# Kernel tuning notes

Hardware: AMD Instinct MI355X
Metric: run time of the kernel (lower is better)

The kernel has to match this reference:

```python
import jax, jax.numpy as jnp
import numpy as np

V = 5000   # vocab (input_size == output_size)
H = 512    # hidden_size
N = 8      # batch
T = 2048   # sequence length


def setup_inputs() -> dict:
    key = jax.random.key(0)
    ks = jax.random.split(key, 6)
    x = jax.random.randint(ks[0], (N, T), 0, V)
    # embedding table (acts as W_xh: xh = E[token])
    E = jax.random.normal(ks[1], (V, H), dtype=jnp.float32) * 0.02
    # hidden Linear(H, H): torch convention W [out, in], y = h @ W.T + b
    Wh = jax.random.normal(ks[2], (H, H), dtype=jnp.float32) * (1.0 / np.sqrt(H))
    bh = jnp.zeros((H,), dtype=jnp.float32)
    # out Linear(H, V)
    Wo = jax.random.normal(ks[3], (V, H), dtype=jnp.float32) * (1.0 / np.sqrt(H))
    bo = jnp.zeros((V,), dtype=jnp.float32)
    return {"x": x, "E": E, "Wh": Wh, "bh": bh, "Wo": Wo, "bo": bo}


def reference(x, E, Wh, bh, Wo, bo):
    n = x.shape[0]
    h0 = jnp.zeros((n, H), dtype=E.dtype)  # h=None -> zeros, broadcast over batch

    def step(h, x_t):
        xh = E[x_t]                              # [N, H] embedding lookup
        h = jnp.tanh(xh + h @ Wh.T + bh)         # [N, H]
        z = h @ Wo.T + bo                        # [N, V]
        return h, jax.nn.softmax(z, axis=-1)

    h_final, y = jax.lax.scan(step, h0, x.T)     # y: [T, N, V]
    return jnp.transpose(y, (1, 0, 2)), h_final  # ([N, T, V], [N, H])
```

## Files before the change

kernel.cpp:

```cpp
#include <hip/hip_runtime.h>
#include <cstdint>
#include <cmath>

#define V_SZ 5000
#define H_SZ 512
#define N_SZ 8
#define T_LEN 2048
#define NTV (81920000LL)

typedef __bf16 bf16;
typedef __bf16 bf16x2 __attribute__((ext_vector_type(2)));
typedef __bf16 bf16x8 __attribute__((ext_vector_type(8)));
typedef float  f32x4  __attribute__((ext_vector_type(4)));
typedef int    i32x4  __attribute__((ext_vector_type(4)));

__device__ __forceinline__ void llc_store16(void* p, i32x4 v) {
    asm volatile("global_store_dwordx4 %0, %1, off sc0 sc1"
                 :: "v"(p), "v"(v) : "memory");
}
__device__ __forceinline__ void llc_load2(const void* p0, const void* p1,
                                          i32x4& a, i32x4& b) {
    asm volatile("global_load_dwordx4 %0, %2, off sc0 sc1\n\t"
                 "global_load_dwordx4 %1, %3, off sc0 sc1\n\t"
                 "s_waitcnt vmcnt(0)"
                 : "=&v"(a), "=&v"(b)
                 : "v"(p0), "v"(p1)
                 : "memory");
}

__global__ __launch_bounds__(256) void prep_wo(const float* __restrict__ Wo,
                                               bf16* __restrict__ Wo16) {
    int idx = (blockIdx.x * 256 + threadIdx.x) * 4;
    if (idx >= 5120 * 512) return;
    float4 v = make_float4(0.f, 0.f, 0.f, 0.f);
    if (idx < V_SZ * H_SZ) v = *(const float4*)(Wo + idx);
    Wo16[idx + 0] = (bf16)v.x;
    Wo16[idx + 1] = (bf16)v.y;
    Wo16[idx + 2] = (bf16)v.z;
    Wo16[idx + 3] = (bf16)v.w;
}

__global__ __launch_bounds__(1024, 1) void rnn_rec3(
        const int*   __restrict__ x,
        const float* __restrict__ E,
        const float* __restrict__ Wh,
        const float* __restrict__ bh,
        char*        __restrict__ Hx,
        bf16*        __restrict__ Hall,
        float*       __restrict__ out) {
    __shared__ bf16  Abuf[2 * 16 * 520];
    __shared__ float Ds[16 * 272];

    const int tid  = threadIdx.x;
    const int blk  = blockIdx.x;
    const int lane = tid & 63;
    const int wv   = tid >> 6;
    const int l15  = lane & 15;
    const int quad = lane >> 4;
    const int j0   = blk * 128;

    for (int i = tid; i < 2 * 16 * 520; i += 1024) Abuf[i] = (bf16)0.f;

    bf16x8 wf[16];
    {
        const float* wrow = Wh + (size_t)(j0 + (wv & 7) * 16 + l15) * H_SZ;
        const bool lo_pass = (wv >= 8);
#pragma unroll
        for (int kt = 0; kt < 16; ++kt) {
            const float* p = wrow + kt * 32 + quad * 8;
            bf16x8 f;
#pragma unroll
            for (int i = 0; i < 8; ++i) {
                float v = p[i];
                bf16 hi = (bf16)v;
                f[i] = lo_pass ? (bf16)(v - (float)hi) : hi;
            }
            wf[kt] = f;
        }
    }

    const int rn = tid >> 7, rj = tid & 127;
    const float bhv = bh[j0 + rj];
    const int jt = rj >> 4, jl = rj & 15;
    const int* xrow = x + rn * T_LEN;

    int off0, off1, dst0, dst1;
    bool has1 = (tid < 512);
    {
        int c0 = tid;
        int rbp0 = c0 >> 9, cc0 = c0 & 511;
        int rb0 = rbp0 + (rbp0 >= blk);
        off0 = (rb0 * 512 + cc0) * 16;
        dst0 = (cc0 >> 6) * 520 + rb0 * 128 + 2 * (cc0 & 63);
        int c1 = has1 ? (tid + 1024) : c0;
        int rbp1 = c1 >> 9, cc1 = c1 & 511;
        int rb1 = rbp1 + (rbp1 >= blk);
        off1 = (rb1 * 512 + cc1) * 16;
        dst1 = (cc1 >> 6) * 520 + rb1 * 128 + 2 * (cc1 & 63);
    }

    int budget = 1 << 22;
    __syncthreads();

    for (int t = 0; t < T_LEN; ++t) {
        const float ev = E[(size_t)xrow[t] * H_SZ + j0 + rj];

        if (t > 0) {
            const char* base = Hx + (size_t)(t & 1) * 32768;
            bf16* An = Abuf + (t & 1) * (16 * 520);
            const int wtag = t;
            const void* p0 = base + off0;
            const void* p1 = base + off1;
            bool need0 = true, need1 = has1;
            while (need0 | need1) {
                i32x4 a, b;
                llc_load2(p0, p1, a, b);
                if (need0 & (a.y == wtag) & (a.w == wtag)) {
                    float h0 = __int_as_float(a.x), h1 = __int_as_float(a.z);
                    bf16 hi0 = (bf16)h0, hi1 = (bf16)h1;
                    *(bf16x2*)(An + dst0) = (bf16x2){hi0, hi1};
                    *(bf16x2*)(An + 8 * 520 + dst0) =
                        (bf16x2){(bf16)(h0 - (float)hi0), (bf16)(h1 - (float)hi1)};
                    need0 = false;
                }
                if (need1 & (b.y == wtag) & (b.w == wtag)) {
                    float h0 = __int_as_float(b.x), h1 = __int_as_float(b.z);
                    bf16 hi0 = (bf16)h0, hi1 = (bf16)h1;
                    *(bf16x2*)(An + dst1) = (bf16x2){hi0, hi1};
                    *(bf16x2*)(An + 8 * 520 + dst1) =
                        (bf16x2){(bf16)(h0 - (float)hi0), (bf16)(h1 - (float)hi1)};
                    need1 = false;
                }
                if (--budget < 0) break;
            }
        }
        __syncthreads();

        {
            const bf16* Ab = Abuf + (t & 1) * (16 * 520);
            f32x4 acc = {}, acc2 = {};
#pragma unroll
            for (int kt = 0; kt < 16; kt += 2) {
                bf16x8 af0 = *(const bf16x8*)(Ab + l15 * 520 + kt * 32 + quad * 8);
                bf16x8 af1 = *(const bf16x8*)(Ab + l15 * 520 + (kt + 1) * 32 + quad * 8);
                acc  = __builtin_amdgcn_mfma_f32_16x16x32_bf16(af0, wf[kt],     acc,  0, 0, 0);
                acc2 = __builtin_amdgcn_mfma_f32_16x16x32_bf16(af1, wf[kt + 1], acc2, 0, 0, 0);
            }
            acc += acc2;
#pragma unroll
            for (int r = 0; r < 4; ++r)
                Ds[wv * 272 + (quad * 4 + r) * 17 + l15] = acc[r];
        }
        __syncthreads();

        {
            float s = Ds[jt * 272 + rn * 17 + jl]
                    + Ds[jt * 272 + (rn + 8) * 17 + jl]
                    + Ds[(jt + 8) * 272 + rn * 17 + jl]
                    + Ds[(jt + 8) * 272 + (rn + 8) * 17 + jl];
            float h = tanhf(s + bhv + ev);

            float hodd = __shfl_xor(h, 1, 64);
            if (((tid & 1) == 0) & (t < T_LEN - 1)) {
                i32x4 ch;
                ch.x = __float_as_int(h);
                ch.y = t + 1;
                ch.z = __float_as_int(hodd);
                ch.w = t + 1;
                char* dstp = Hx + (size_t)((t + 1) & 1) * 32768
                           + (size_t)(blk * 512 + rn * 64 + (rj >> 1)) * 16;
                llc_store16(dstp, ch);
            }

            Hall[((size_t)rn * T_LEN + t) * H_SZ + j0 + rj] = (bf16)h;
            bf16 hi = (bf16)h;
            bf16* An = Abuf + ((t + 1) & 1) * (16 * 520);
            An[rn * 520 + j0 + rj] = hi;
            An[(rn + 8) * 520 + j0 + rj] = (bf16)(h - (float)hi);
            if (t == T_LEN - 1) out[NTV + rn * H_SZ + j0 + rj] = h;
        }
    }
}

#define LDK 72
__global__ __launch_bounds__(256) void gemm_bt(
        const bf16* __restrict__ A,
        const bf16* __restrict__ B,
        const float* __restrict__ bo,
        float* __restrict__ C) {
    __shared__ bf16 As[128 * LDK];
    __shared__ bf16 Bs[128 * LDK];

    const int tid  = threadIdx.x;
    const int lane = tid & 63;
    const int wid  = tid >> 6;
    const int wm   = wid & 1, wn = wid >> 1;
    const int bm   = blockIdx.y, bn = blockIdx.x;
    const int rowA0 = bm * 128, rowB0 = bn * 128;

    const int quad = lane >> 4;
    const int l15  = lane & 15;

    f32x4 acc[4][4] = {};

    for (int kt = 0; kt < H_SZ / 64; ++kt) {
        __syncthreads();
#pragma unroll
        for (int i = 0; i < 4; ++i) {
            int p = i * 256 + tid;
            int r = p >> 3, c8 = p & 7;
            bf16x8 va = *(const bf16x8*)(A + (size_t)(rowA0 + r) * H_SZ + kt * 64 + c8 * 8);
            *(bf16x8*)(As + r * LDK + c8 * 8) = va;
            bf16x8 vb = *(const bf16x8*)(B + (size_t)(rowB0 + r) * H_SZ + kt * 64 + c8 * 8);
            *(bf16x8*)(Bs + r * LDK + c8 * 8) = vb;
        }
        __syncthreads();

#pragma unroll
        for (int ks = 0; ks < 2; ++ks) {
            bf16x8 af[4], bfr[4];
            const int koff = ks * 32 + quad * 8;
#pragma unroll
            for (int mi = 0; mi < 4; ++mi) {
                int row = wm * 64 + mi * 16 + l15;
                af[mi] = *(const bf16x8*)(As + row * LDK + koff);
            }
#pragma unroll
            for (int ni = 0; ni < 4; ++ni) {
                int row = wn * 64 + ni * 16 + l15;
                bfr[ni] = *(const bf16x8*)(Bs + row * LDK + koff);
            }
#pragma unroll
            for (int mi = 0; mi < 4; ++mi)
#pragma unroll
                for (int ni = 0; ni < 4; ++ni)
                    acc[mi][ni] = __builtin_amdgcn_mfma_f32_16x16x32_bf16(
                        af[mi], bfr[ni], acc[mi][ni], 0, 0, 0);
        }
    }

#pragma unroll
    for (int mi = 0; mi < 4; ++mi) {
#pragma unroll
        for (int ni = 0; ni < 4; ++ni) {
            int vcol = rowB0 + wn * 64 + ni * 16 + l15;
            if (vcol >= V_SZ) continue;
            float bias = bo[vcol];
#pragma unroll
            for (int r = 0; r < 4; ++r) {
                int m = rowA0 + wm * 64 + mi * 16 + quad * 4 + r;
                C[(size_t)m * V_SZ + vcol] = acc[mi][ni][r] + bias;
            }
        }
    }
}

__global__ __launch_bounds__(256) void softmax_rows(float* __restrict__ z) {
    __shared__ float buf[5008];
    __shared__ float red[8];
    const int tid = threadIdx.x;
    const int lane = tid & 63;
    const int wid = tid >> 6;
    const size_t base = (size_t)blockIdx.x * V_SZ;

    float lm = -3.4e38f;
    for (int i = tid; i < V_SZ; i += 256) {
        float v = z[base + i];
        buf[i] = v;
        lm = fmaxf(lm, v);
    }
#pragma unroll
    for (int o = 32; o; o >>= 1) lm = fmaxf(lm, __shfl_down(lm, o, 64));
    if (lane == 0) red[wid] = lm;
    __syncthreads();
    const float m = fmaxf(fmaxf(red[0], red[1]), fmaxf(red[2], red[3]));

    float ls = 0.f;
    for (int i = tid; i < V_SZ; i += 256) {
        float e = __expf(buf[i] - m);
        buf[i] = e;
        ls += e;
    }
#pragma unroll
    for (int o = 32; o; o >>= 1) ls += __shfl_down(ls, o, 64);
    __syncthreads();
    if (lane == 0) red[4 + wid] = ls;
    __syncthreads();
    const float inv = 1.0f / (red[4] + red[5] + red[6] + red[7]);
    for (int i = tid; i < V_SZ; i += 256) z[base + i] = buf[i] * inv;
}

extern "C" void kernel_launch(void* const* d_in, const int* in_sizes, int n_in,
                              void* d_out, int out_size, void* d_ws, size_t ws_size,
                              hipStream_t stream) {
    const int*   x  = (const int*)d_in[0];
    const float* E  = (const float*)d_in[1];
    const float* Wh = (const float*)d_in[2];
    const float* bh = (const float*)d_in[3];
    const float* Wo = (const float*)d_in[4];
    const float* bo = (const float*)d_in[5];
    float* out = (float*)d_out;

    char* ws = (char*)d_ws;
    char*  Hx   = ws;
    bf16*  Wo16 = (bf16*)(ws + 65536);
    bf16*  Hall = (bf16*)(ws + 8388608);

    prep_wo<<<2560, 256, 0, stream>>>(Wo, Wo16);
    rnn_rec3<<<4, 1024, 0, stream>>>(x, E, Wh, bh, Hx, Hall, out);
    gemm_bt<<<dim3(40, 128), 256, 0, stream>>>(Hall, Wo16, bo, out);
    softmax_rows<<<16384, 256, 0, stream>>>(out);
}
```

Before: 6.279 ms.

## Pipeline cross-block hidden-state polling with three in-flight probe loads

Replaces the blocking load-and-wait spin loop with a rotating set of three outstanding probe loads, so each check waits only for the oldest probe and polling latency overlaps with the next loads. It also replaces __syncthreads with an LDS-only wait plus a raw barrier, which avoids draining outstanding global memory ops, and caches the token indices in shared memory to shorten the dependent embedding load. Hand-written vmcnt accounting is fragile: leftover in-flight probes from earlier steps and the other global loads and stores may break the assumed counts or reorder memory visibility.

```diff
diff --git a/kernel.cpp b/kernel.cpp
--- a/kernel.cpp
+++ b/kernel.cpp
@@ -18,14 +18,23 @@
     asm volatile("global_store_dwordx4 %0, %1, off sc0 sc1"
                  :: "v"(p), "v"(v) : "memory");
 }
-__device__ __forceinline__ void llc_load2(const void* p0, const void* p1,
-                                          i32x4& a, i32x4& b) {
+__device__ __forceinline__ void probe_issue(const void* p0, const void* p1,
+                                            i32x4& a, i32x4& b) {
     asm volatile("global_load_dwordx4 %0, %2, off sc0 sc1\n\t"
-                 "global_load_dwordx4 %1, %3, off sc0 sc1\n\t"
-                 "s_waitcnt vmcnt(0)"
+                 "global_load_dwordx4 %1, %3, off sc0 sc1"
                  : "=&v"(a), "=&v"(b)
                  : "v"(p0), "v"(p1)
                  : "memory");
+}
+__device__ __forceinline__ void probe_wait4(i32x4& a, i32x4& b) {
+    asm volatile("s_waitcnt vmcnt(4)" : "+v"(a), "+v"(b) :: "memory");
+    __builtin_amdgcn_sched_barrier(0);
+}
+__device__ __forceinline__ void bar_lds() {
+    asm volatile("s_waitcnt lgkmcnt(0)" ::: "memory");
+    __builtin_amdgcn_sched_barrier(0);
+    __builtin_amdgcn_s_barrier();
+    __builtin_amdgcn_sched_barrier(0);
 }
 
 __global__ __launch_bounds__(256) void prep_wo(const float* __restrict__ Wo,
@@ -50,6 +59,7 @@
         float*       __restrict__ out) {
     __shared__ bf16  Abuf[2 * 16 * 520];
     __shared__ float Ds[16 * 272];
+    __shared__ int   tokT[8 * T_LEN];
 
     const int tid  = threadIdx.x;
     const int blk  = blockIdx.x;
@@ -60,6 +70,8 @@
     const int j0   = blk * 128;
 
     for (int i = tid; i < 2 * 16 * 520; i += 1024) Abuf[i] = (bf16)0.f;
+    for (int i = tid; i < (8 * T_LEN) / 4; i += 1024)
+        ((int4*)tokT)[i] = ((const int4*)x)[i];
 
     bf16x8 wf[16];
     {
@@ -82,7 +94,6 @@
     const int rn = tid >> 7, rj = tid & 127;
     const float bhv = bh[j0 + rj];
     const int jt = rj >> 4, jl = rj & 15;
-    const int* xrow = x + rn * T_LEN;
 
     int off0, off1, dst0, dst1;
     bool has1 = (tid < 512);
@@ -99,11 +110,32 @@
         dst1 = (cc1 >> 6) * 520 + rb1 * 128 + 2 * (cc1 & 63);
     }
 
+    i32x4 qa0 = {}, qb0 = {}, qa1 = {}, qb1 = {}, qa2 = {}, qb2 = {};
     int budget = 1 << 22;
     __syncthreads();
 
+#define SPIN_CHECK(qa, qb)                                                    \
+    do {                                                                      \
+        if (need0 & ((qa).y == wtag) & ((qa).w == wtag)) {                    \
+            float h0 = __int_as_float((qa).x), h1 = __int_as_float((qa).z);   \
+            bf16 hi0 = (bf16)h0, hi1 = (bf16)h1;                              \
+            *(bf16x2*)(An + dst0) = (bf16x2){hi0, hi1};                       \
+            *(bf16x2*)(An + 8 * 520 + dst0) =                                 \
+                (bf16x2){(bf16)(h0 - (float)hi0), (bf16)(h1 - (float)hi1)};   \
+            need0 = false;                                                    \
+        }                                                                     \
+        if (need1 & ((qb).y == wtag) & ((qb).w == wtag)) {                    \
+            float h0 = __int_as_float((qb).x), h1 = __int_as_float((qb).z);   \
+            bf16 hi0 = (bf16)h0, hi1 = (bf16)h1;                              \
+            *(bf16x2*)(An + dst1) = (bf16x2){hi0, hi1};                       \
+            *(bf16x2*)(An + 8 * 520 + dst1) =                                 \
+                (bf16x2){(bf16)(h0 - (float)hi0), (bf16)(h1 - (float)hi1)};   \
+            need1 = false;                                                    \
+        }                                                                     \
+    } while (0)
+
     for (int t = 0; t < T_LEN; ++t) {
-        const float ev = E[(size_t)xrow[t] * H_SZ + j0 + rj];
+        const float ev = E[(size_t)tokT[rn * T_LEN + t] * H_SZ + j0 + rj];
 
         if (t > 0) {
             const char* base = Hx + (size_t)(t & 1) * 32768;
@@ -112,29 +144,31 @@
             const void* p0 = base + off0;
             const void* p1 = base + off1;
             bool need0 = true, need1 = has1;
-            while (need0 | need1) {
-                i32x4 a, b;
-                llc_load2(p0, p1, a, b);
-                if (need0 & (a.y == wtag) & (a.w == wtag)) {
-                    float h0 = __int_as_float(a.x), h1 = __int_as_float(a.z);
-                    bf16 hi0 = (bf16)h0, hi1 = (bf16)h1;
-                    *(bf16x2*)(An + dst0) = (bf16x2){hi0, hi1};
-                    *(bf16x2*)(An + 8 * 520 + dst0) =
-                        (bf16x2){(bf16)(h0 - (float)hi0), (bf16)(h1 - (float)hi1)};
-                    need0 = false;
-                }
-                if (need1 & (b.y == wtag) & (b.w == wtag)) {
-                    float h0 = __int_as_float(b.x), h1 = __int_as_float(b.z);
-                    bf16 hi0 = (bf16)h0, hi1 = (bf16)h1;
-                    *(bf16x2*)(An + dst1) = (bf16x2){hi0, hi1};
-                    *(bf16x2*)(An + 8 * 520 + dst1) =
-                        (bf16x2){(bf16)(h0 - (float)hi0), (bf16)(h1 - (float)hi1)};
-                    need1 = false;
-                }
+            asm volatile("s_waitcnt vmcnt(3)" ::: "memory");
+            probe_issue(p0, p1, qa0, qb0);
+            probe_issue(p0, p1, qa1, qb1);
+            probe_issue(p0, p1, qa2, qb2);
+            for (;;) {
+                probe_wait4(qa0, qb0);
+                SPIN_CHECK(qa0, qb0);
+                if (!(need0 | need1)) break;
+                probe_issue(p0, p1, qa0, qb0);
                 if (--budget < 0) break;
-            }
-        }
-        __syncthreads();
+
+                probe_wait4(qa1, qb1);
+                SPIN_CHECK(qa1, qb1);
+                if (!(need0 | need1)) break;
+                probe_issue(p0, p1, qa1, qb1);
+                if (--budget < 0) break;
+
+                probe_wait4(qa2, qb2);
+                SPIN_CHECK(qa2, qb2);
+                if (!(need0 | need1)) break;
+                probe_issue(p0, p1, qa2, qb2);
+                if (--budget < 0) break;
+            }
+        }
+        bar_lds();
 
         {
             const bf16* Ab = Abuf + (t & 1) * (16 * 520);
@@ -151,7 +185,7 @@
             for (int r = 0; r < 4; ++r)
                 Ds[wv * 272 + (quad * 4 + r) * 17 + l15] = acc[r];
         }
-        __syncthreads();
+        bar_lds();
 
         {
             float s = Ds[jt * 272 + rn * 17 + jl]
@@ -179,7 +213,10 @@
             An[(rn + 8) * 520 + j0 + rj] = (bf16)(h - (float)hi);
             if (t == T_LEN - 1) out[NTV + rn * H_SZ + j0 + rj] = h;
         }
-    }
+        asm volatile("" :: "v"(qa0), "v"(qb0), "v"(qa1), "v"(qb1),
+                           "v"(qa2), "v"(qb2));
+    }
+#undef SPIN_CHECK
 }
 
 #define LDK 72
```

New measurement: 11.23 ms. 1.79x slower.

## Halve recurrence block to 512 threads, keeping hi/lo weights per wave

Applied to the files above, without the earlier changes.

The recurrent kernel now uses 512 threads per block, and each wave holds both the hi and lo bf16 splits of its Wh slice. This removes the shared-memory partial-sum reduction and one __syncthreads per timestep; the cross-split sum is done with a lane shuffle. Hidden values are exchanged between blocks already packed as bf16 hi/lo pairs, so receivers copy them straight into LDS without converting. The embedding lookup for the next step is prefetched after the current step's stores. The cost is higher register pressure (32 weight fragments per thread) and three polling loads per thread instead of two.

```diff
diff --git a/kernel.cpp b/kernel.cpp
--- a/kernel.cpp
+++ b/kernel.cpp
@@ -18,13 +18,15 @@
     asm volatile("global_store_dwordx4 %0, %1, off sc0 sc1"
                  :: "v"(p), "v"(v) : "memory");
 }
-__device__ __forceinline__ void llc_load2(const void* p0, const void* p1,
-                                          i32x4& a, i32x4& b) {
-    asm volatile("global_load_dwordx4 %0, %2, off sc0 sc1\n\t"
-                 "global_load_dwordx4 %1, %3, off sc0 sc1\n\t"
+__device__ __forceinline__ void llc_load3(const void* p0, const void* p1,
+                                          const void* p2,
+                                          i32x4& a, i32x4& b, i32x4& c) {
+    asm volatile("global_load_dwordx4 %0, %3, off sc0 sc1\n\t"
+                 "global_load_dwordx4 %1, %4, off sc0 sc1\n\t"
+                 "global_load_dwordx4 %2, %5, off sc0 sc1\n\t"
                  "s_waitcnt vmcnt(0)"
-                 : "=&v"(a), "=&v"(b)
-                 : "v"(p0), "v"(p1)
+                 : "=&v"(a), "=&v"(b), "=&v"(c)
+                 : "v"(p0), "v"(p1), "v"(p2)
                  : "memory");
 }
 
@@ -40,7 +42,7 @@
     Wo16[idx + 3] = (bf16)v.w;
 }
 
-__global__ __launch_bounds__(1024, 1) void rnn_rec3(
+__global__ __launch_bounds__(512, 2) void rnn_rec4(
         const int*   __restrict__ x,
         const float* __restrict__ E,
         const float* __restrict__ Wh,
@@ -48,136 +50,161 @@
         char*        __restrict__ Hx,
         bf16*        __restrict__ Hall,
         float*       __restrict__ out) {
-    __shared__ bf16  Abuf[2 * 16 * 520];
-    __shared__ float Ds[16 * 272];
+    __shared__ bf16 Abuf[2 * 16 * 520];
 
     const int tid  = threadIdx.x;
     const int blk  = blockIdx.x;
     const int lane = tid & 63;
-    const int wv   = tid >> 6;
+    const int w    = tid >> 6;
     const int l15  = lane & 15;
     const int quad = lane >> 4;
     const int j0   = blk * 128;
-
-    for (int i = tid; i < 2 * 16 * 520; i += 1024) Abuf[i] = (bf16)0.f;
-
-    bf16x8 wf[16];
+    const int jcol = w * 16 + l15;
+    const int jglob = j0 + jcol;
+
+    for (int i = tid; i < 2 * 16 * 520; i += 512) Abuf[i] = (bf16)0.f;
+
+    bf16x8 wfh[16], wfl[16];
     {
-        const float* wrow = Wh + (size_t)(j0 + (wv & 7) * 16 + l15) * H_SZ;
-        const bool lo_pass = (wv >= 8);
+        const float* wrow = Wh + (size_t)(j0 + w * 16 + l15) * H_SZ;
 #pragma unroll
         for (int kt = 0; kt < 16; ++kt) {
             const float* p = wrow + kt * 32 + quad * 8;
-            bf16x8 f;
+            bf16x8 fh, fl;
 #pragma unroll
             for (int i = 0; i < 8; ++i) {
                 float v = p[i];
                 bf16 hi = (bf16)v;
-                f[i] = lo_pass ? (bf16)(v - (float)hi) : hi;
-            }
-            wf[kt] = f;
-        }
-    }
-
-    const int rn = tid >> 7, rj = tid & 127;
-    const float bhv = bh[j0 + rj];
-    const int jt = rj >> 4, jl = rj & 15;
-    const int* xrow = x + rn * T_LEN;
-
-    int off0, off1, dst0, dst1;
-    bool has1 = (tid < 512);
+                fh[i] = hi;
+                fl[i] = (bf16)(v - (float)hi);
+            }
+            wfh[kt] = fh;
+            wfl[kt] = fl;
+        }
+    }
+
+    const int n0 = (quad & 1) * 4 + (quad >> 1) * 2;
+    const int n1 = n0 + 1;
+    const bool hiHalf = (quad >> 1) != 0;
+    const float bhv = bh[jglob];
+    const int* xr0 = x + n0 * T_LEN;
+    const int* xr1 = x + n1 * T_LEN;
+
+    int off0, off1, off2, dst0, dst1, dst2;
     {
-        int c0 = tid;
-        int rbp0 = c0 >> 9, cc0 = c0 & 511;
-        int rb0 = rbp0 + (rbp0 >= blk);
-        off0 = (rb0 * 512 + cc0) * 16;
-        dst0 = (cc0 >> 6) * 520 + rb0 * 128 + 2 * (cc0 & 63);
-        int c1 = has1 ? (tid + 1024) : c0;
-        int rbp1 = c1 >> 9, cc1 = c1 & 511;
-        int rb1 = rbp1 + (rbp1 >= blk);
-        off1 = (rb1 * 512 + cc1) * 16;
-        dst1 = (cc1 >> 6) * 520 + rb1 * 128 + 2 * (cc1 & 63);
-    }
+        int c, rbp, cc, rb;
+        c = tid;          rbp = c >> 9; cc = c & 511; rb = rbp + (rbp >= blk);
+        off0 = (rb * 512 + cc) * 16; dst0 = (cc >> 6) * 520 + rb * 128 + 2 * (cc & 63);
+        c = tid + 512;    rbp = c >> 9; cc = c & 511; rb = rbp + (rbp >= blk);
+        off1 = (rb * 512 + cc) * 16; dst1 = (cc >> 6) * 520 + rb * 128 + 2 * (cc & 63);
+        c = tid + 1024;   rbp = c >> 9; cc = c & 511; rb = rbp + (rbp >= blk);
+        off2 = (rb * 512 + cc) * 16; dst2 = (cc >> 6) * 520 + rb * 128 + 2 * (cc & 63);
+    }
+
+    float ev0 = E[(size_t)xr0[0] * H_SZ + jglob];
+    float ev1 = E[(size_t)xr1[0] * H_SZ + jglob];
 
     int budget = 1 << 22;
     __syncthreads();
 
     for (int t = 0; t < T_LEN; ++t) {
-        const float ev = E[(size_t)xrow[t] * H_SZ + j0 + rj];
-
         if (t > 0) {
             const char* base = Hx + (size_t)(t & 1) * 32768;
             bf16* An = Abuf + (t & 1) * (16 * 520);
             const int wtag = t;
             const void* p0 = base + off0;
             const void* p1 = base + off1;
-            bool need0 = true, need1 = has1;
-            while (need0 | need1) {
-                i32x4 a, b;
-                llc_load2(p0, p1, a, b);
-                if (need0 & (a.y == wtag) & (a.w == wtag)) {
-                    float h0 = __int_as_float(a.x), h1 = __int_as_float(a.z);
-                    bf16 hi0 = (bf16)h0, hi1 = (bf16)h1;
-                    *(bf16x2*)(An + dst0) = (bf16x2){hi0, hi1};
-                    *(bf16x2*)(An + 8 * 520 + dst0) =
-                        (bf16x2){(bf16)(h0 - (float)hi0), (bf16)(h1 - (float)hi1)};
-                    need0 = false;
+            const void* p2 = base + off2;
+            bool q0 = true, q1 = true, q2 = true;
+            while (q0 | q1 | q2) {
+                i32x4 a, b, c3;
+                llc_load3(p0, p1, p2, a, b, c3);
+                if (q0 & (a.y == wtag) & (a.w == wtag)) {
+                    *(int*)(An + dst0) = a.x;
+                    *(int*)(An + 8 * 520 + dst0) = a.z;
+                    q0 = false;
                 }
-                if (need1 & (b.y == wtag) & (b.w == wtag)) {
-                    float h0 = __int_as_float(b.x), h1 = __int_as_float(b.z);
-                    bf16 hi0 = (bf16)h0, hi1 = (bf16)h1;
-                    *(bf16x2*)(An + dst1) = (bf16x2){hi0, hi1};
-                    *(bf16x2*)(An + 8 * 520 + dst1) =
-                        (bf16x2){(bf16)(h0 - (float)hi0), (bf16)(h1 - (float)hi1)};
-                    need1 = false;
+                if (q1 & (b.y == wtag) & (b.w == wtag)) {
+                    *(int*)(An + dst1) = b.x;
+                    *(int*)(An + 8 * 520 + dst1) = b.z;
+                    q1 = false;
+                }
+                if (q2 & (c3.y == wtag) & (c3.w == wtag)) {
+                    *(int*)(An + dst2) = c3.x;
+                    *(int*)(An + 8 * 520 + dst2) = c3.z;
+                    q2 = false;
                 }
                 if (--budget < 0) break;
             }
         }
         __syncthreads();
 
+        f32x4 sp;
         {
             const bf16* Ab = Abuf + (t & 1) * (16 * 520);
-            f32x4 acc = {}, acc2 = {};
+            f32x4 c0 = {}, c1 = {}, c2 = {}, c3 = {};
 #pragma unroll
             for (int kt = 0; kt < 16; kt += 2) {
                 bf16x8 af0 = *(const bf16x8*)(Ab + l15 * 520 + kt * 32 + quad * 8);
                 bf16x8 af1 = *(const bf16x8*)(Ab + l15 * 520 + (kt + 1) * 32 + quad * 8);
-                acc  = __builtin_amdgcn_mfma_f32_16x16x32_bf16(af0, wf[kt],     acc,  0, 0, 0);
-                acc2 = __builtin_amdgcn_mfma_f32_16x16x32_bf16(af1, wf[kt + 1], acc2, 0, 0, 0);
-            }
-            acc += acc2;
-#pragma unroll
-            for (int r = 0; r < 4; ++r)
-                Ds[wv * 272 + (quad * 4 + r) * 17 + l15] = acc[r];
-        }
-        __syncthreads();
+                c0 = __builtin_amdgcn_mfma_f32_16x16x32_bf16(af0, wfh[kt],     c0, 0, 0, 0);
+                c1 = __builtin_amdgcn_mfma_f32_16x16x32_bf16(af0, wfl[kt],     c1, 0, 0, 0);
+                c2 = __builtin_amdgcn_mfma_f32_16x16x32_bf16(af1, wfh[kt + 1], c2, 0, 0, 0);
+                c3 = __builtin_amdgcn_mfma_f32_16x16x32_bf16(af1, wfl[kt + 1], c3, 0, 0, 0);
+            }
+            sp = (c0 + c2) + (c1 + c3);
+        }
 
         {
-            float s = Ds[jt * 272 + rn * 17 + jl]
-                    + Ds[jt * 272 + (rn + 8) * 17 + jl]
-                    + Ds[(jt + 8) * 272 + rn * 17 + jl]
-                    + Ds[(jt + 8) * 272 + (rn + 8) * 17 + jl];
-            float h = tanhf(s + bhv + ev);
-
-            float hodd = __shfl_xor(h, 1, 64);
-            if (((tid & 1) == 0) & (t < T_LEN - 1)) {
-                i32x4 ch;
-                ch.x = __float_as_int(h);
-                ch.y = t + 1;
-                ch.z = __float_as_int(hodd);
-                ch.w = t + 1;
+            float mA = hiHalf ? sp[2] : sp[0];
+            float mB = hiHalf ? sp[3] : sp[1];
+            float xA = hiHalf ? sp[0] : sp[2];
+            float xB = hiHalf ? sp[1] : sp[3];
+            float s0 = mA + __shfl_xor(xA, 32, 64);
+            float s1 = mB + __shfl_xor(xB, 32, 64);
+
+            float h0 = tanhf(s0 + bhv + ev0);
+            float h1 = tanhf(s1 + bhv + ev1);
+
+            bf16 hi0 = (bf16)h0;  bf16 lo0 = (bf16)(h0 - (float)hi0);
+            bf16 hi1 = (bf16)h1;  bf16 lo1 = (bf16)(h1 - (float)hi1);
+            bf16x2 pr0 = {hi0, lo0};  int pk0 = __builtin_bit_cast(int, pr0);
+            bf16x2 pr1 = {hi1, lo1};  int pk1 = __builtin_bit_cast(int, pr1);
+            int nb0 = __shfl_xor(pk0, 1, 64);
+            int nb1 = __shfl_xor(pk1, 1, 64);
+
+            if (t < T_LEN - 1) {
+                const bool oddl = (l15 & 1);
+                int dwhi = oddl ? ((nb1 & 0xFFFF) | ((pk1 & 0xFFFF) << 16))
+                                : ((pk0 & 0xFFFF) | (nb0 << 16));
+                int dwlo = oddl ? ((int)((unsigned)nb1 >> 16) | (pk1 & 0xFFFF0000))
+                                : ((int)((unsigned)pk0 >> 16) | (nb0 & 0xFFFF0000));
+                int cn   = oddl ? n1 : n0;
+                int jp   = (w << 3) + (l15 >> 1);
+                i32x4 ch = {dwhi, t + 1, dwlo, t + 1};
                 char* dstp = Hx + (size_t)((t + 1) & 1) * 32768
-                           + (size_t)(blk * 512 + rn * 64 + (rj >> 1)) * 16;
+                           + (size_t)(blk * 512 + cn * 64 + jp) * 16;
                 llc_store16(dstp, ch);
             }
 
-            Hall[((size_t)rn * T_LEN + t) * H_SZ + j0 + rj] = (bf16)h;
-            bf16 hi = (bf16)h;
             bf16* An = Abuf + ((t + 1) & 1) * (16 * 520);
-            An[rn * 520 + j0 + rj] = hi;
-            An[(rn + 8) * 520 + j0 + rj] = (bf16)(h - (float)hi);
-            if (t == T_LEN - 1) out[NTV + rn * H_SZ + j0 + rj] = h;
+            An[n0 * 520 + jglob] = hi0;
+            An[(n0 + 8) * 520 + jglob] = lo0;
+            An[n1 * 520 + jglob] = hi1;
+            An[(n1 + 8) * 520 + jglob] = lo1;
+
+            Hall[((size_t)n0 * T_LEN + t) * H_SZ + jglob] = hi0;
+            Hall[((size_t)n1 * T_LEN + t) * H_SZ + jglob] = hi1;
+
+            if (t + 1 < T_LEN) {
+                ev0 = E[(size_t)xr0[t + 1] * H_SZ + jglob];
+                ev1 = E[(size_t)xr1[t + 1] * H_SZ + jglob];
+            }
+
+            if (t == T_LEN - 1) {
+                out[NTV + n0 * H_SZ + jglob] = h0;
+                out[NTV + n1 * H_SZ + jglob] = h1;
+            }
         }
     }
 }
@@ -307,7 +334,7 @@
     bf16*  Hall = (bf16*)(ws + 8388608);
 
     prep_wo<<<2560, 256, 0, stream>>>(Wo, Wo16);
-    rnn_rec3<<<4, 1024, 0, stream>>>(x, E, Wh, bh, Hx, Hall, out);
+    rnn_rec4<<<4, 512, 0, stream>>>(x, E, Wh, bh, Hx, Hall, out);
     gemm_bt<<<dim3(40, 128), 256, 0, stream>>>(Hall, Wo16, bo, out);
     softmax_rows<<<16384, 256, 0, stream>>>(out);
 }
```

Measured after the change: 5.032 ms. -19.9%, faster.
